# Kernel optimization log

Measured on AMD Instinct MI355X. Metric: run time of the kernel, lower is better.

Reference implementation:

```python
import math
import jax, jax.numpy as jnp
import numpy as np

B, N, D = 8, 2048, 512


def setup_inputs() -> dict:
    key = jax.random.key(0)
    ks = jax.random.split(key, 9)
    s = 1.0 / math.sqrt(D)
    return {
        "x": jax.random.normal(ks[0], (B, N, D), dtype=jnp.float32),
        "adj": jax.random.uniform(ks[1], (B, N, N), dtype=jnp.float32),
        "Wqk": jax.random.normal(ks[2], (D, D), dtype=jnp.float32) * s,
        "bqk": jax.random.normal(ks[3], (D,), dtype=jnp.float32) * s,
        "Wl": jax.random.normal(ks[4], (D, D), dtype=jnp.float32) * s,
        "bl": jax.random.normal(ks[5], (D,), dtype=jnp.float32) * s,
        "Wr": jax.random.normal(ks[6], (D, D), dtype=jnp.float32) * s,
        "Wd": jax.random.normal(ks[7], (D, 1), dtype=jnp.float32),
        "bd": jax.random.normal(ks[8], (D,), dtype=jnp.float32),
    }


def reference(x, adj, Wqk, bqk, Wl, bl, Wr, Wd, bd):
    # degree gating: sigmoid(Linear(rowsum(adj)))
    deg = jnp.sum(adj, axis=-1, keepdims=True)           # [B, N, 1]
    gate = jax.nn.sigmoid(deg * Wd[:, 0] + bd)           # [B, N, D]
    xg = x * gate
    # sigmoid QK features
    QK = jax.nn.sigmoid(xg @ Wqk.T + bqk)                # [B, N, D]
    scores = jnp.einsum("bnd,bmd->bnm", QK, QK) / math.sqrt(D)
    scores = scores * adj                                # adjacency mask
    attn = scores / (jnp.sum(scores, axis=-1, keepdims=True) + 1e-6)
    out = jnp.einsum("bnm,bmd->bnd", attn, xg)           # aggregate values
    out = out @ Wl.T + bl + xg @ Wr.T                    # left + right branch
    return jax.nn.relu(out)
```

## Files before the change

### kernel.cpp

```cpp
#include <hip/hip_runtime.h>
#include <hip/hip_bf16.h>


typedef __bf16 bf16;
typedef __bf16 bf16x2 __attribute__((ext_vector_type(2)));
typedef __bf16 bf16x8 __attribute__((ext_vector_type(8)));
typedef float  f32x4  __attribute__((ext_vector_type(4)));

#define Bb 8
#define Nn 2048
#define Dd 512
#define TILE8_BYTES 49152
#define SMEM8_BYTES (3 * TILE8_BYTES)
#define ATTN_SMEM 147456

__device__ __forceinline__ bf16 to_bf16(float f) { return (bf16)f; }
__device__ __forceinline__ float sigmoidf_(float x) { return 1.0f / (1.0f + __expf(-x)); }

__device__ __forceinline__ void gld16(const void* g, void* l) {
    __builtin_amdgcn_global_load_lds(
        (__attribute__((address_space(1))) void*)(void*)g,
        (__attribute__((address_space(3))) void*)l,
        16, 0, 0);
}

__device__ __forceinline__ void gemm_bt8_core(
    const bf16* __restrict__ A0, const bf16* __restrict__ B0,
    int lda0, int ldb0, int nt0,
    const bf16* __restrict__ A1, const bf16* __restrict__ B1,
    int lda1, int ldb1, int nt1,
    char* smem, f32x4 acc[4][4])
{
    const int tid  = threadIdx.x;
    const int lane = tid & 63;
    const int wave = tid >> 6;
    const int wm = (wave >> 1) << 6;
    const int wn = (wave & 1) << 6;
    const int NT = nt0 + nt1;

    char* bA = smem;
    char* bB = smem + TILE8_BYTES;
    char* bC = smem + 2 * TILE8_BYTES;

    auto stage_tile = [&](char* base, int t) {
        const bf16* A  = (t < nt0) ? A0 : A1;
        const bf16* Bt = (t < nt0) ? B0 : B1;
        const int lda  = (t < nt0) ? lda0 : lda1;
        const int ldb  = (t < nt0) ? ldb0 : ldb1;
        const int kt   = ((t < nt0) ? t : t - nt0) << 6;
#pragma unroll
        for (int i = 0; i < 4; ++i) {
            int ff   = i * 512 + tid;
            int row  = ff >> 3;
            int slot = ff & 7;
            int gch  = slot ^ (row & 7);
            gld16(A + (size_t)row * lda + kt + gch * 8, base + ff * 16);
        }
#pragma unroll
        for (int i = 0; i < 2; ++i) {
            int ff   = i * 512 + tid;
            int row  = ff >> 3;
            int slot = ff & 7;
            int gch  = slot ^ (row & 7);
            gld16(Bt + (size_t)row * ldb + kt + gch * 8, base + 32768 + ff * 16);
        }
    };

    stage_tile(bA, 0);
    stage_tile(bB, 1);
    asm volatile("s_waitcnt vmcnt(6)" ::: "memory");
    __builtin_amdgcn_s_barrier();

#pragma unroll 1
    for (int t = 0; t < NT; ++t) {
        bf16x8 af0[4], bf0[4], af1[4], bf1[4];
#pragma unroll
        for (int mi = 0; mi < 4; ++mi) {
            int row  = wm + mi * 16 + (lane & 15);
            int slot = (lane >> 4) ^ (row & 7);
            af0[mi] = *(const bf16x8*)(bA + row * 128 + slot * 16);
        }
#pragma unroll
        for (int ni = 0; ni < 4; ++ni) {
            int row  = wn + ni * 16 + (lane & 15);
            int slot = (lane >> 4) ^ (row & 7);
            bf0[ni] = *(const bf16x8*)(bA + 32768 + row * 128 + slot * 16);
        }
        if (t + 2 < NT) stage_tile(bC, t + 2);
        __builtin_amdgcn_s_barrier();
        asm volatile("s_waitcnt lgkmcnt(0)" ::: "memory");
        __builtin_amdgcn_sched_barrier(0);
#pragma unroll
        for (int mi = 0; mi < 4; ++mi) {
            int row  = wm + mi * 16 + (lane & 15);
            int slot = (4 + (lane >> 4)) ^ (row & 7);
            af1[mi] = *(const bf16x8*)(bA + row * 128 + slot * 16);
        }
#pragma unroll
        for (int ni = 0; ni < 4; ++ni) {
            int row  = wn + ni * 16 + (lane & 15);
            int slot = (4 + (lane >> 4)) ^ (row & 7);
            bf1[ni] = *(const bf16x8*)(bA + 32768 + row * 128 + slot * 16);
        }
        __builtin_amdgcn_sched_barrier(0);
        __builtin_amdgcn_s_setprio(1);
#pragma unroll
        for (int mi = 0; mi < 4; ++mi)
#pragma unroll
            for (int ni = 0; ni < 4; ++ni)
                acc[mi][ni] = __builtin_amdgcn_mfma_f32_16x16x32_bf16(
                    af0[mi], bf0[ni], acc[mi][ni], 0, 0, 0);
        __builtin_amdgcn_s_setprio(0);
        asm volatile("s_waitcnt lgkmcnt(0)" ::: "memory");
        __builtin_amdgcn_sched_barrier(0);
        __builtin_amdgcn_s_setprio(1);
#pragma unroll
        for (int mi = 0; mi < 4; ++mi)
#pragma unroll
            for (int ni = 0; ni < 4; ++ni)
                acc[mi][ni] = __builtin_amdgcn_mfma_f32_16x16x32_bf16(
                    af1[mi], bf1[ni], acc[mi][ni], 0, 0, 0);
        __builtin_amdgcn_s_setprio(0);
        __builtin_amdgcn_sched_barrier(0);
        if (t + 2 < NT)      asm volatile("s_waitcnt vmcnt(6)" ::: "memory");
        else if (t + 1 < NT) asm volatile("s_waitcnt vmcnt(0)" ::: "memory");
        __builtin_amdgcn_s_barrier();
        char* tmp = bA; bA = bB; bB = bC; bC = tmp;
    }
}

template <typename F>
__device__ __forceinline__ void epilogue_rt8(f32x4 acc[4][4], char* smem, F&& emit)
{
    const int tid  = threadIdx.x;
    const int lane = tid & 63;
    const int wave = tid >> 6;
    const int wm4 = wave >> 1;
    const int wn  = (wave & 1) << 6;
    const int cq = lane >> 4;
    const int cl = lane & 15;
    float* t = (float*)smem;
    const int chunk = tid & 15;
    const int rbase = tid >> 4;
#pragma unroll
    for (int ph = 0; ph < 4; ++ph) {
        __syncthreads();
        if (wm4 == ph) {
#pragma unroll
            for (int mi = 0; mi < 4; ++mi)
#pragma unroll
                for (int ni = 0; ni < 4; ++ni)
#pragma unroll
                    for (int r = 0; r < 4; ++r) {
                        int lr = mi * 16 + cq * 4 + r;
                        int lc = wn + ni * 16 + cl;
                        t[lr * 132 + lc] = acc[mi][ni][r];
                    }
        }
        __syncthreads();
#pragma unroll
        for (int rr = 0; rr < 2; ++rr) {
            int lr = rr * 32 + rbase;
            f32x4 a = *(const f32x4*)&t[lr * 132 + chunk * 8];
            f32x4 b = *(const f32x4*)&t[lr * 132 + chunk * 8 + 4];
            float v[8] = {a[0], a[1], a[2], a[3], b[0], b[1], b[2], b[3]};
            emit(ph * 64 + lr, chunk * 8, v);
        }
    }
}

__global__ __launch_bounds__(256) void k_gate(
    const float* __restrict__ x, const float* __restrict__ adj,
    const float* __restrict__ Wd, const float* __restrict__ bd,
    const float* __restrict__ Wqk, const float* __restrict__ Wl,
    const float* __restrict__ Wr,
    bf16* __restrict__ xg, bf16* __restrict__ Wqkb, bf16* __restrict__ Wlb,
    bf16* __restrict__ Wrb)
{
    const int rowg = blockIdx.x;
    const int tid  = threadIdx.x;
    if (tid < 48) {
        int idx = rowg * 48 + tid;
        if (idx < 262144)      Wqkb[idx]          = to_bf16(Wqk[idx]);
        else if (idx < 524288) Wlb[idx - 262144]  = to_bf16(Wl[idx - 262144]);
        else                   Wrb[idx - 524288]  = to_bf16(Wr[idx - 524288]);
    }

    const float4* arow = (const float4*)(adj + (size_t)rowg * Nn);
    float4 v0 = arow[tid];
    float4 v1 = arow[tid + 256];
    float s = v0.x + v0.y + v0.z + v0.w + v1.x + v1.y + v1.z + v1.w;
#pragma unroll
    for (int off = 32; off > 0; off >>= 1) s += __shfl_down(s, off, 64);
    __shared__ float red[4];
    if ((tid & 63) == 0) red[tid >> 6] = s;
    __syncthreads();
    const float deg = red[0] + red[1] + red[2] + red[3];
    const int d2 = tid;
    float2 xv  = ((const float2*)(x + (size_t)rowg * Dd))[d2];
    float2 wd  = ((const float2*)Wd)[d2];
    float2 bd2 = ((const float2*)bd)[d2];
    bf16x2 o;
    o[0] = to_bf16(xv.x * sigmoidf_(deg * wd.x + bd2.x));
    o[1] = to_bf16(xv.y * sigmoidf_(deg * wd.y + bd2.y));
    *(bf16x2*)(xg + (size_t)rowg * Dd + d2 * 2) = o;
}

__global__ __launch_bounds__(256) void k_transpose(
    const bf16* __restrict__ xg, bf16* __restrict__ xgT)
{
    const int b = blockIdx.z, nt = blockIdx.y, dt = blockIdx.x;
    __shared__ bf16 tile[64][66];
    const int c = threadIdx.x & 63, r0 = threadIdx.x >> 6;
    const bf16* src = xg + ((size_t)b * Nn + nt * 64) * Dd + dt * 64;
#pragma unroll
    for (int i = 0; i < 16; ++i) {
        int r = i * 4 + r0;
        tile[r][c] = src[(size_t)r * Dd + c];
    }
    __syncthreads();
    bf16* dst = xgT + ((size_t)b * Dd + dt * 64) * Nn + nt * 64;
#pragma unroll
    for (int i = 0; i < 16; ++i) {
        int r = i * 4 + r0;
        dst[(size_t)r * Nn + c] = tile[c][r];
    }
}

__global__ __launch_bounds__(512) void k_qk_gemm8(
    const bf16* __restrict__ xg, const bf16* __restrict__ Wqkb,
    const float* __restrict__ bqk, bf16* __restrict__ QK)
{
    extern __shared__ __align__(16) char smem[];
    const int blockRow = blockIdx.y * 256;
    const int blockCol = blockIdx.x * 128;
    f32x4 acc[4][4];
#pragma unroll
    for (int mi = 0; mi < 4; ++mi)
#pragma unroll
        for (int ni = 0; ni < 4; ++ni) acc[mi][ni] = (f32x4){0.f, 0.f, 0.f, 0.f};
    gemm_bt8_core(xg + (size_t)blockRow * Dd, Wqkb + (size_t)blockCol * Dd,
                  Dd, Dd, 8,
                  xg, Wqkb, Dd, Dd, 0, smem, acc);
    epilogue_rt8(acc, smem, [&](int lr, int lc, float* v) {
        int c = blockCol + lc;
        float4 b0 = *(const float4*)(bqk + c);
        float4 b1 = *(const float4*)(bqk + c + 4);
        float bb[8] = {b0.x, b0.y, b0.z, b0.w, b1.x, b1.y, b1.z, b1.w};
        bf16x8 o;
#pragma unroll
        for (int j = 0; j < 8; ++j) o[j] = to_bf16(sigmoidf_(v[j] + bb[j]));
        *(bf16x8*)(QK + (size_t)(blockRow + lr) * Dd + c) = o;
    });
}

__global__ __launch_bounds__(512, 2) void k_attn(
    const bf16* __restrict__ QK, const bf16* __restrict__ xgT,
    const float* __restrict__ adj, bf16* __restrict__ h)
{
    extern __shared__ __align__(16) char smem[];
    char* qki = smem;
    char* Pl  = smem + 65536;
    char* adj0 = smem + 81920;
    char* adj1 = smem + 114688;
    float* dred = (float*)adj0;
    float* dinv = (float*)(adj0 + 2048);

    const int id   = blockIdx.x;
    const int b    = id & 7;
    const int row0 = (id >> 3) * 64;
    const int tid  = threadIdx.x;
    const int lane = tid & 63, w = tid >> 6;
    const int cq = lane >> 4, cl = lane & 15;

    const bf16*  QKb  = QK  + (size_t)b * Nn * Dd;
    const bf16*  QKi  = QKb + (size_t)row0 * Dd;
    const bf16*  xgTb = xgT + (size_t)b * Dd * Nn;
    const float* adjb = adj + (size_t)b * Nn * Nn + (size_t)row0 * Nn;

    auto stage_adj = [&](char* base, int jt) {
        const int j0 = jt << 7;
#pragma unroll
        for (int i = 0; i < 4; ++i) {
            int ff  = i * 512 + tid;
            int row = ff >> 5, slot = ff & 31;
            int gch = (slot & 24) | ((slot & 7) ^ (row & 7));
            gld16(adjb + (size_t)row * Nn + j0 + gch * 4, base + ff * 16);
        }
    };

#pragma unroll
    for (int i = 0; i < 8; ++i) {
        int ff = i * 512 + tid;
        int row = ff >> 6, slot = ff & 63;
        int gch = (slot & 56) | ((slot & 7) ^ (row & 7));
        gld16(QKi + (size_t)row * Dd + gch * 8, qki + ff * 16);
    }
    stage_adj(adj0, 0);

    f32x4 hacc[4][4];
#pragma unroll
    for (int mi = 0; mi < 4; ++mi)
#pragma unroll
        for (int ni = 0; ni < 4; ++ni) hacc[mi][ni] = (f32x4){0.f, 0.f, 0.f, 0.f};
    float dloc[16];
#pragma unroll
    for (int i = 0; i < 16; ++i) dloc[i] = 0.f;

    __syncthreads();

    const float scale = 0.044194173824159216f;

#pragma unroll 1
    for (int jt = 0; jt < 16; ++jt) {
        const int j0 = jt << 7;
        f32x4 tacc[4];
#pragma unroll
        for (int mi = 0; mi < 4; ++mi) tacc[mi] = (f32x4){0.f, 0.f, 0.f, 0.f};
#pragma unroll
        for (int kc = 0; kc < 16; ++kc) {
            bf16x8 bq = *(const bf16x8*)(QKb
                + (size_t)(j0 + w * 16 + cl) * Dd + kc * 32 + cq * 8);
            bf16x8 af[4];
#pragma unroll
            for (int mi = 0; mi < 4; ++mi) {
                int i = mi * 16 + cl;
                int c = kc * 4 + cq;
                int ph = (c & 56) | ((c & 7) ^ (i & 7));
                af[mi] = *(const bf16x8*)(qki + i * 1024 + ph * 16);
            }
#pragma unroll
            for (int mi = 0; mi < 4; ++mi)
                tacc[mi] = __builtin_amdgcn_mfma_f32_16x16x32_bf16(
                    af[mi], bq, tacc[mi], 0, 0, 0);
        }
        __syncthreads();

        const char* ab = (jt & 1) ? adj1 : adj0;
#pragma unroll
        for (int mi = 0; mi < 4; ++mi)
#pragma unroll
            for (int r = 0; r < 4; ++r) {
                int i = mi * 16 + cq * 4 + r;
                int ca = w * 4 + (cl >> 2);
                int pha = (ca & 24) | ((ca & 7) ^ (i & 7));
                float a = *(const float*)(ab + i * 512 + pha * 16 + (cl & 3) * 4);
                float s = tacc[mi][r] * scale * a;
                bf16 sb = to_bf16(s);
                int cj = w * 2 + (cl >> 3);
                int phj = (cj & 8) | ((cj & 7) ^ (i & 7));
                *(bf16*)(Pl + i * 256 + phj * 16 + (cl & 7) * 2) = sb;
                dloc[mi * 4 + r] += (float)sb;
            }
        if (jt + 1 < 16) stage_adj((jt & 1) ? adj0 : adj1, jt + 1);
        asm volatile("s_waitcnt lgkmcnt(0)" ::: "memory");
        __builtin_amdgcn_sched_barrier(0);
        __builtin_amdgcn_s_barrier();

#pragma unroll
        for (int kc = 0; kc < 4; ++kc) {
            bf16x8 pa[4], xb[4];
#pragma unroll
            for (int mi = 0; mi < 4; ++mi) {
                int i = mi * 16 + cl;
                int c = kc * 4 + cq;
                int ph = (c & 8) | ((c & 7) ^ (i & 7));
                pa[mi] = *(const bf16x8*)(Pl + i * 256 + ph * 16);
            }
#pragma unroll
            for (int ni = 0; ni < 4; ++ni)
                xb[ni] = *(const bf16x8*)(xgTb
                    + (size_t)(w * 64 + ni * 16 + cl) * Nn + j0 + kc * 32 + cq * 8);
#pragma unroll
            for (int mi = 0; mi < 4; ++mi)
#pragma unroll
                for (int ni = 0; ni < 4; ++ni)
                    hacc[mi][ni] = __builtin_amdgcn_mfma_f32_16x16x32_bf16(
                        pa[mi], xb[ni], hacc[mi][ni], 0, 0, 0);
        }
    }

#pragma unroll
    for (int i = 0; i < 16; ++i)
#pragma unroll
        for (int off = 1; off < 16; off <<= 1)
            dloc[i] += __shfl_xor(dloc[i], off, 64);
    if (cl == 0) {
#pragma unroll
        for (int mi = 0; mi < 4; ++mi)
#pragma unroll
            for (int r = 0; r < 4; ++r)
                dred[w * 64 + mi * 16 + cq * 4 + r] = dloc[mi * 4 + r];
    }
    __syncthreads();
    if (tid < 64) {
        float s = 0.f;
#pragma unroll
        for (int k = 0; k < 8; ++k) s += dred[k * 64 + tid];
        dinv[tid] = 1.0f / (s + 1e-6f);
    }
    __syncthreads();

    float* hs = (float*)smem;
#pragma unroll
    for (int p = 0; p < 2; ++p) {
        if (p) __syncthreads();
#pragma unroll
        for (int m2 = 0; m2 < 2; ++m2) {
            int mi = p * 2 + m2;
#pragma unroll
            for (int r = 0; r < 4; ++r) {
                float iv = dinv[mi * 16 + cq * 4 + r];
                int lrow = m2 * 16 + cq * 4 + r;
#pragma unroll
                for (int ni = 0; ni < 4; ++ni)
                    hs[lrow * 516 + w * 64 + ni * 16 + cl] = hacc[mi][ni][r] * iv;
            }
        }
        __syncthreads();
        {
            int row = tid & 31, ch = tid >> 5;
            int grow = row0 + p * 32 + row;
            bf16* dst = h + ((size_t)b * Nn + grow) * Dd + ch * 32;
            const float* src = hs + row * 516 + ch * 32;
#pragma unroll
            for (int g = 0; g < 4; ++g) {
                f32x4 u = *(const f32x4*)(src + g * 8);
                f32x4 q = *(const f32x4*)(src + g * 8 + 4);
                bf16x8 o;
                o[0] = to_bf16(u[0]); o[1] = to_bf16(u[1]);
                o[2] = to_bf16(u[2]); o[3] = to_bf16(u[3]);
                o[4] = to_bf16(q[0]); o[5] = to_bf16(q[1]);
                o[6] = to_bf16(q[2]); o[7] = to_bf16(q[3]);
                *(bf16x8*)(dst + g * 8) = o;
            }
        }
    }
}

__global__ __launch_bounds__(512) void k_out_gemm8(
    const bf16* __restrict__ h, const bf16* __restrict__ xg,
    const bf16* __restrict__ Wlb, const bf16* __restrict__ Wrb,
    const float* __restrict__ bl, float* __restrict__ out)
{
    extern __shared__ __align__(16) char smem[];
    const int blockRow = blockIdx.y * 256;
    const int blockCol = blockIdx.x * 128;
    f32x4 acc[4][4];
#pragma unroll
    for (int mi = 0; mi < 4; ++mi)
#pragma unroll
        for (int ni = 0; ni < 4; ++ni) acc[mi][ni] = (f32x4){0.f, 0.f, 0.f, 0.f};
    gemm_bt8_core(h  + (size_t)blockRow * Dd, Wlb + (size_t)blockCol * Dd,
                  Dd, Dd, 8,
                  xg + (size_t)blockRow * Dd, Wrb + (size_t)blockCol * Dd,
                  Dd, Dd, 8, smem, acc);
    epilogue_rt8(acc, smem, [&](int lr, int lc, float* v) {
        int c = blockCol + lc;
        float4 b0 = *(const float4*)(bl + c);
        float4 b1 = *(const float4*)(bl + c + 4);
        float bb[8] = {b0.x, b0.y, b0.z, b0.w, b1.x, b1.y, b1.z, b1.w};
        float4 o0, o1;
        o0.x = fmaxf(v[0] + bb[0], 0.f); o0.y = fmaxf(v[1] + bb[1], 0.f);
        o0.z = fmaxf(v[2] + bb[2], 0.f); o0.w = fmaxf(v[3] + bb[3], 0.f);
        o1.x = fmaxf(v[4] + bb[4], 0.f); o1.y = fmaxf(v[5] + bb[5], 0.f);
        o1.z = fmaxf(v[6] + bb[6], 0.f); o1.w = fmaxf(v[7] + bb[7], 0.f);
        float* p = out + (size_t)(blockRow + lr) * Dd + c;
        *(float4*)p = o0;
        *(float4*)(p + 4) = o1;
    });
}

extern "C" void kernel_launch(void* const* d_in, const int* in_sizes, int n_in,
                              void* d_out, int out_size, void* d_ws, size_t ws_size,
                              hipStream_t stream) {
    const float* x   = (const float*)d_in[0];
    const float* adj = (const float*)d_in[1];
    const float* Wqk = (const float*)d_in[2];
    const float* bqk = (const float*)d_in[3];
    const float* Wl  = (const float*)d_in[4];
    const float* bl  = (const float*)d_in[5];
    const float* Wr  = (const float*)d_in[6];
    const float* Wd  = (const float*)d_in[7];
    const float* bd  = (const float*)d_in[8];
    float* out = (float*)d_out;

    char* ws = (char*)d_ws;
    bf16* xg   = (bf16*)ws;  ws += (size_t)Bb * Nn * Dd * 2;
    bf16* xgT  = (bf16*)ws;  ws += (size_t)Bb * Dd * Nn * 2;
    bf16* QK   = (bf16*)ws;  ws += (size_t)Bb * Nn * Dd * 2;
    bf16* h    = (bf16*)ws;  ws += (size_t)Bb * Nn * Dd * 2;
    bf16* Wqkb = (bf16*)ws;  ws += (size_t)Dd * Dd * 2;
    bf16* Wlb  = (bf16*)ws;  ws += (size_t)Dd * Dd * 2;
    bf16* Wrb  = (bf16*)ws;  ws += (size_t)Dd * Dd * 2;

    static bool attr_done = false;
    if (!attr_done) {
        hipFuncSetAttribute((const void*)k_qk_gemm8,
                            hipFuncAttributeMaxDynamicSharedMemorySize, SMEM8_BYTES);
        hipFuncSetAttribute((const void*)k_attn,
                            hipFuncAttributeMaxDynamicSharedMemorySize, ATTN_SMEM);
        hipFuncSetAttribute((const void*)k_out_gemm8,
                            hipFuncAttributeMaxDynamicSharedMemorySize, SMEM8_BYTES);
        attr_done = true;
    }

    k_gate<<<dim3(Bb * Nn), 256, 0, stream>>>(x, adj, Wd, bd, Wqk, Wl, Wr,
                                              xg, Wqkb, Wlb, Wrb);
    k_transpose<<<dim3(Dd / 64, Nn / 64, Bb), 256, 0, stream>>>(xg, xgT);
    k_qk_gemm8<<<dim3(Dd / 128, (Bb * Nn) / 256), 512, SMEM8_BYTES, stream>>>(xg, Wqkb, bqk, QK);
    k_attn<<<dim3(256), 512, ATTN_SMEM, stream>>>(QK, xgT, adj, h);
    k_out_gemm8<<<dim3(Dd / 128, (Bb * Nn) / 256), 512, SMEM8_BYTES, stream>>>(h, xg, Wlb, Wrb, bl, out);
}
```

Baseline: 440.0 us.

## Stage adjacency tiles through registers instead of LDS to raise attention occupancy

Removes the double-buffered LDS staging of adjacency tiles and instead prefetches each thread's adjacency values for the next column tile directly into registers during the current tile. This cuts the attention kernel's shared memory from about 144 KB to 80 KB, so more blocks can fit per CU, and launch bounds are raised to ask for 4 blocks. The reduction scratch now aliases the P buffer, so an extra barrier is added before it is reused. The tighter launch bound may force heavy register spilling, and the per-thread scalar adjacency loads are narrower than the previous 16-byte async copies.

Result: slower. 646.4 us (+46.9%).

```diff
diff --git a/kernel.cpp b/kernel.cpp
--- a/kernel.cpp
+++ b/kernel.cpp
@@ -12,7 +12,7 @@
 #define Dd 512
 #define TILE8_BYTES 49152
 #define SMEM8_BYTES (3 * TILE8_BYTES)
-#define ATTN_SMEM 147456
+#define ATTN_SMEM 81920
 
 __device__ __forceinline__ bf16 to_bf16(float f) { return (bf16)f; }
 __device__ __forceinline__ float sigmoidf_(float x) { return 1.0f / (1.0f + __expf(-x)); }
@@ -254,17 +254,15 @@
     });
 }
 
-__global__ __launch_bounds__(512, 2) void k_attn(
+__global__ __launch_bounds__(512, 4) void k_attn(
     const bf16* __restrict__ QK, const bf16* __restrict__ xgT,
     const float* __restrict__ adj, bf16* __restrict__ h)
 {
     extern __shared__ __align__(16) char smem[];
     char* qki = smem;
     char* Pl  = smem + 65536;
-    char* adj0 = smem + 81920;
-    char* adj1 = smem + 114688;
-    float* dred = (float*)adj0;
-    float* dinv = (float*)(adj0 + 2048);
+    float* dred = (float*)Pl;
+    float* dinv = (float*)(Pl + 2048);
 
     const int id   = blockIdx.x;
     const int b    = id & 7;
@@ -278,17 +276,6 @@
     const bf16*  xgTb = xgT + (size_t)b * Dd * Nn;
     const float* adjb = adj + (size_t)b * Nn * Nn + (size_t)row0 * Nn;
 
-    auto stage_adj = [&](char* base, int jt) {
-        const int j0 = jt << 7;
-#pragma unroll
-        for (int i = 0; i < 4; ++i) {
-            int ff  = i * 512 + tid;
-            int row = ff >> 5, slot = ff & 31;
-            int gch = (slot & 24) | ((slot & 7) ^ (row & 7));
-            gld16(adjb + (size_t)row * Nn + j0 + gch * 4, base + ff * 16);
-        }
-    };
-
 #pragma unroll
     for (int i = 0; i < 8; ++i) {
         int ff = i * 512 + tid;
@@ -296,7 +283,6 @@
         int gch = (slot & 56) | ((slot & 7) ^ (row & 7));
         gld16(QKi + (size_t)row * Dd + gch * 8, qki + ff * 16);
     }
-    stage_adj(adj0, 0);
 
     f32x4 hacc[4][4];
 #pragma unroll
@@ -306,6 +292,14 @@
     float dloc[16];
 #pragma unroll
     for (int i = 0; i < 16; ++i) dloc[i] = 0.f;
+
+    float adjc[16];
+#pragma unroll
+    for (int mi = 0; mi < 4; ++mi)
+#pragma unroll
+        for (int r = 0; r < 4; ++r)
+            adjc[mi * 4 + r] =
+                adjb[(size_t)(mi * 16 + cq * 4 + r) * Nn + w * 16 + cl];
 
     __syncthreads();
 
@@ -336,23 +330,27 @@
         }
         __syncthreads();
 
-        const char* ab = (jt & 1) ? adj1 : adj0;
 #pragma unroll
         for (int mi = 0; mi < 4; ++mi)
 #pragma unroll
             for (int r = 0; r < 4; ++r) {
                 int i = mi * 16 + cq * 4 + r;
-                int ca = w * 4 + (cl >> 2);
-                int pha = (ca & 24) | ((ca & 7) ^ (i & 7));
-                float a = *(const float*)(ab + i * 512 + pha * 16 + (cl & 3) * 4);
-                float s = tacc[mi][r] * scale * a;
+                float s = tacc[mi][r] * scale * adjc[mi * 4 + r];
                 bf16 sb = to_bf16(s);
                 int cj = w * 2 + (cl >> 3);
                 int phj = (cj & 8) | ((cj & 7) ^ (i & 7));
                 *(bf16*)(Pl + i * 256 + phj * 16 + (cl & 7) * 2) = sb;
                 dloc[mi * 4 + r] += (float)sb;
             }
-        if (jt + 1 < 16) stage_adj((jt & 1) ? adj0 : adj1, jt + 1);
+        if (jt + 1 < 16) {
+#pragma unroll
+            for (int mi = 0; mi < 4; ++mi)
+#pragma unroll
+                for (int r = 0; r < 4; ++r)
+                    adjc[mi * 4 + r] =
+                        adjb[(size_t)(mi * 16 + cq * 4 + r) * Nn
+                             + (j0 + 128) + w * 16 + cl];
+        }
         asm volatile("s_waitcnt lgkmcnt(0)" ::: "memory");
         __builtin_amdgcn_sched_barrier(0);
         __builtin_amdgcn_s_barrier();
@@ -379,6 +377,8 @@
                         pa[mi], xb[ni], hacc[mi][ni], 0, 0, 0);
         }
     }
+
+    __syncthreads();
 
 #pragma unroll
     for (int i = 0; i < 16; ++i)
```
